# Kernel tuning notes

Measured on AMD Instinct MI355X. Metric: run time of the kernel, lower is better.

## Reference

```python
import jax, jax.numpy as jnp
import numpy as np

B, S, IN, H, D, STATE, PRED = 256, 512, 32, 256, 32, 4, 96


def setup_inputs() -> dict:
    key = jax.random.key(0)
    ks = jax.random.split(key, 16)
    sc = 1.0 / np.sqrt(H)

    def u(k, shape):
        return jax.random.uniform(k, shape, jnp.float32, -sc, sc)

    return {
        "x": jax.random.normal(ks[0], (B, S, IN), jnp.float32),
        # GRU layer 0
        "W_ih_l0": u(ks[1], (3 * H, IN)),
        "W_hh_l0": u(ks[2], (3 * H, H)),
        "b_ih_l0": u(ks[3], (3 * H,)),
        "b_hh_l0": u(ks[4], (3 * H,)),
        # GRU layer 1
        "W_ih_l1": u(ks[5], (3 * H, H)),
        "W_hh_l1": u(ks[6], (3 * H, H)),
        "b_ih_l1": u(ks[7], (3 * H,)),
        "b_hh_l1": u(ks[8], (3 * H,)),
        # state projection: hidden -> STATE*output_dim
        "W_proj": u(ks[9], (STATE * D, H)),
        "b_proj": u(ks[10], (STATE * D,)),
        # observation matrix, eye-initialized (output_dim, STATE)
        "C": jnp.eye(D, STATE, dtype=jnp.float32),
        "raw_level_decay": jnp.zeros((D,), jnp.float32),
        "raw_trend_decay": jnp.zeros((D,), jnp.float32),
        "raw_gamma": jnp.zeros((D,), jnp.float32),
        "omega": jnp.zeros((D,), jnp.float32),
    }


def _gru_layer(xs, W_ih, W_hh, b_ih, b_hh):
    # xs: (B, S, in_dim). Precompute input projections as one big GEMM.
    xp = jnp.einsum('bsi,gi->bsg', xs, W_ih) + b_ih  # (B, S, 3H)

    def step(h, xt):
        gh = h @ W_hh.T + b_hh  # (B, 3H)
        xr, xz, xn = jnp.split(xt, 3, axis=-1)
        hr, hz, hn = jnp.split(gh, 3, axis=-1)
        r = jax.nn.sigmoid(xr + hr)
        z = jax.nn.sigmoid(xz + hz)
        n = jnp.tanh(xn + r * hn)
        h_new = (1.0 - z) * n + z * h
        return h_new, h_new

    h0 = jnp.zeros((xs.shape[0], W_hh.shape[1]), xs.dtype)
    _, hs = jax.lax.scan(step, h0, jnp.swapaxes(xp, 0, 1))  # (S, B, H)
    return jnp.swapaxes(hs, 0, 1)  # (B, S, H)


def reference(x, W_ih_l0, W_hh_l0, b_ih_l0, b_hh_l0,
              W_ih_l1, W_hh_l1, b_ih_l1, b_hh_l1,
              W_proj, b_proj, C,
              raw_level_decay, raw_trend_decay, raw_gamma, omega):
    h1 = _gru_layer(x, W_ih_l0, W_hh_l0, b_ih_l0, b_hh_l0)
    h2 = _gru_layer(h1, W_ih_l1, W_hh_l1, b_ih_l1, b_hh_l1)
    final_h = h2[:, -1, :]  # (B, H)

    d_out = C.shape[0]
    s = (final_h @ W_proj.T + b_proj).reshape(x.shape[0], d_out, STATE)  # (B, D, 4)

    # time-invariant block-diagonal transition coefficients
    a_l = jax.nn.sigmoid(raw_level_decay) * 0.15 + 0.85
    a_t = jax.nn.sigmoid(raw_trend_decay) * 0.25 + 0.7
    g = jax.nn.sigmoid(raw_gamma) * 0.2 + 0.8
    c, sn = jnp.cos(omega), jnp.sin(omega)
    rot00, rot01 = g * c, -g * sn
    rot10, rot11 = g * sn, g * c

    def step(s, _):
        new_s = jnp.stack([
            s[..., 0] * a_l,
            s[..., 1] * a_t,
            s[..., 2] * rot00 + s[..., 3] * rot10,
            s[..., 2] * rot01 + s[..., 3] * rot11,
        ], axis=-1)
        y = jnp.einsum('ds,bds->bd', C, new_s)
        return new_s, y

    _, ys = jax.lax.scan(step, s, None, length=PRED)  # (PRED, B, D)
    return jnp.swapaxes(ys, 0, 1)  # (B, PRED, D)
```

## Files before the change

### kernel.cpp

```cpp
#include <hip/hip_runtime.h>
#include <cstdio>
#include <cstdint>

typedef _Float16 f16;
typedef f16 hf2   __attribute__((ext_vector_type(2)));
typedef f16 f16x8 __attribute__((ext_vector_type(8)));
typedef float f32x4 __attribute__((ext_vector_type(4)));
typedef unsigned int   u32;
typedef unsigned short u16;

#define B_    256
#define S_    512
#define IN_   32
#define H_    256
#define G3_   768
#define D_    32
#define PRED_ 96
#define TC_   32

#if __has_builtin(__builtin_amdgcn_fdot2)
__device__ __forceinline__ float fdot2(hf2 a, hf2 b, float c) {
  return __builtin_amdgcn_fdot2(a, b, c, false);
}
#else
__device__ __forceinline__ float fdot2(hf2 a, hf2 b, float c) {
  return c + (float)a[0] * (float)b[0] + (float)a[1] * (float)b[1];
}
#endif

__device__ __forceinline__ float sigm(float x) {
  return __builtin_amdgcn_rcpf(1.f + __expf(-x));
}
__device__ __forceinline__ float tanh_fast(float x) {
  return 1.f - 2.f * __builtin_amdgcn_rcpf(__expf(2.f * x) + 1.f);
}
__device__ __forceinline__ hf2 bc2(u32 v) { return __builtin_bit_cast(hf2, v); }

__global__ void f32_to_f16_k(const float* __restrict__ in, f16* __restrict__ out, int n) {
  int i = blockIdx.x * blockDim.x + threadIdx.x;
  if (i < n) out[i] = (f16)in[i];
}

__global__ void make_bias(const float* __restrict__ bih, const float* __restrict__ bhh,
                          float* __restrict__ out) {
  int i = blockIdx.x * blockDim.x + threadIdx.x;
  if (i < G3_) out[i] = bih[i] + (i < 512 ? bhh[i] : 0.f);
}

__device__ __forceinline__ f16x8 cvt8(const float* p) {
  float4 lo = ((const float4*)p)[0];
  float4 hi = ((const float4*)p)[1];
  f16x8 r;
  r[0] = (f16)lo.x; r[1] = (f16)lo.y; r[2] = (f16)lo.z; r[3] = (f16)lo.w;
  r[4] = (f16)hi.x; r[5] = (f16)hi.y; r[6] = (f16)hi.z; r[7] = (f16)hi.w;
  return r;
}

template <int KK>
__global__ __launch_bounds__(256) void gemm_xp(
    const void* __restrict__ Asrc, size_t aBlk, int tl_rows,
    const f16* __restrict__ Wih,
    const float* __restrict__ biasc,
    u16* __restrict__ xp) {
  const int tid = threadIdx.x;
  const int wv = tid >> 6, lane = tid & 63, lm = lane & 15, q = lane >> 4;
  const int tiles_pb = tl_rows >> 6;
  const int b = blockIdx.x / tiles_pb, hf = blockIdx.x % tiles_pb;
  const size_t arow0 = (size_t)b * aBlk + (size_t)(hf * 64) * KK;
  const size_t orow0 = (size_t)b * tl_rows + hf * 64;

#pragma unroll 1
  for (int nt = 0; nt < 12; ++nt) {
    const int n0 = wv * 192 + nt * 16;
    const f16* Bp = Wih + (size_t)(n0 + lm) * KK + q * 8;
    f32x4 acc[4];
#pragma unroll
    for (int j = 0; j < 4; ++j) acc[j] = f32x4{0.f, 0.f, 0.f, 0.f};
#pragma unroll
    for (int k0 = 0; k0 < KK; k0 += 32) {
      f16x8 bv = *(const f16x8*)(Bp + k0);
#pragma unroll
      for (int j = 0; j < 4; ++j) {
        f16x8 av;
        if constexpr (KK == 32) {
          av = cvt8((const float*)Asrc + arow0 + (size_t)(j * 16 + lm) * KK + k0 + q * 8);
        } else {
          av = *(const f16x8*)((const f16*)Asrc + arow0 + (size_t)(j * 16 + lm) * KK + k0 + q * 8);
        }
        acc[j] = __builtin_amdgcn_mfma_f32_16x16x32_f16(av, bv, acc[j], 0, 0, 0);
      }
    }
    const float bb = biasc[n0 + lm];
#pragma unroll
    for (int j = 0; j < 4; ++j)
#pragma unroll
      for (int r = 0; r < 4; ++r)
        xp[(orow0 + j * 16 + q * 4 + r) * G3_ + n0 + lm] =
            __builtin_bit_cast(u16, (f16)(acc[j][r] + bb));
  }
}

template <int LAYER>
__global__ __launch_bounds__(512, 2) void gru_rec(
    const u16* __restrict__ xp,
    const f16* __restrict__ Whh16,
    const float* __restrict__ bhh,
    float* __restrict__ hstate,
    f16* __restrict__ h1c,
    int tl_rows, int first) {
  const int b   = blockIdx.x;
  const int tid = threadIdx.x;
  const int p = tid >> 1, kh = tid & 1;

  uint4 w[48];
  const uint4* wsrc = (const uint4*)Whh16 + (size_t)p * 32 + kh * 16;
#pragma unroll
  for (int g = 0; g < 3; ++g)
#pragma unroll
    for (int u = 0; u < 16; ++u)
      w[g * 16 + u] = wsrc[g * 8192 + u];
  const float bhn = bhh[512 + p];

  __shared__ u16 xbuf[2][TC_ * G3_];
  __shared__ __align__(16) u16 hbuf[2][H_];
  __shared__ u16 hhist[TC_ * H_];

  float h = first ? 0.f : hstate[b * H_ + p];
  if (kh == 0) hbuf[0][p] = __builtin_bit_cast(u16, (f16)h);
  int cur = 0;
  const uint4* xsrc = (const uint4*)xp + (size_t)b * tl_rows * 96;
  const int nsub = tl_rows >> 5;

#pragma unroll 1
  for (int c2 = 0; c2 < nsub; ++c2) {
    {
      const uint4* src = xsrc + (size_t)c2 * 3072;
      uint4 v0 = src[tid],        v1 = src[512 + tid],  v2 = src[1024 + tid];
      uint4 v3 = src[1536 + tid], v4 = src[2048 + tid], v5 = src[2560 + tid];
      uint4* dst = (uint4*)xbuf[c2 & 1];
      dst[tid] = v0;        dst[512 + tid] = v1;  dst[1024 + tid] = v2;
      dst[1536 + tid] = v3; dst[2048 + tid] = v4; dst[2560 + tid] = v5;
    }
    __syncthreads();
    const u16* xrow0 = xbuf[c2 & 1];

#pragma unroll 1
    for (int tl = 0; tl < TC_; ++tl) {
      const uint4* hb = (const uint4*)(hbuf[cur] + kh * 128);
      float ar = 0.f, az = 0.f, an = 0.f, ar2 = 0.f, az2 = 0.f, an2 = 0.f;
#pragma unroll
      for (int cc = 0; cc < 16; ++cc) {
        uint4 hv = hb[cc];
        uint4 w0 = w[cc], w1 = w[16 + cc], w2 = w[32 + cc];
        ar  = fdot2(bc2(w0.x), bc2(hv.x), ar);
        az  = fdot2(bc2(w1.x), bc2(hv.x), az);
        an  = fdot2(bc2(w2.x), bc2(hv.x), an);
        ar2 = fdot2(bc2(w0.y), bc2(hv.y), ar2);
        az2 = fdot2(bc2(w1.y), bc2(hv.y), az2);
        an2 = fdot2(bc2(w2.y), bc2(hv.y), an2);
        ar  = fdot2(bc2(w0.z), bc2(hv.z), ar);
        az  = fdot2(bc2(w1.z), bc2(hv.z), az);
        an  = fdot2(bc2(w2.z), bc2(hv.z), an);
        ar2 = fdot2(bc2(w0.w), bc2(hv.w), ar2);
        az2 = fdot2(bc2(w1.w), bc2(hv.w), az2);
        an2 = fdot2(bc2(w2.w), bc2(hv.w), an2);
      }
      ar += ar2; az += az2; an += an2;
      ar += __shfl_xor(ar, 1);
      az += __shfl_xor(az, 1);
      an += __shfl_xor(an, 1);

      const u16* xrow = xrow0 + tl * G3_;
      float xr = (float)__builtin_bit_cast(f16, xrow[p]);
      float xz = (float)__builtin_bit_cast(f16, xrow[256 + p]);
      float xn = (float)__builtin_bit_cast(f16, xrow[512 + p]);
      float r = sigm(xr + ar);
      float z = sigm(xz + az);
      float n = tanh_fast(xn + r * (an + bhn));
      h = n + z * (h - n);

      if (kh == 0) {
        u16 h16v = __builtin_bit_cast(u16, (f16)h);
        hbuf[cur ^ 1][p] = h16v;
        if constexpr (LAYER == 0) hhist[tl * H_ + p] = h16v;
      }
      __syncthreads();
      cur ^= 1;
    }

    if constexpr (LAYER == 0) {
      uint4 hv0 = ((const uint4*)hhist)[tid];
      uint4 hv1 = ((const uint4*)hhist)[512 + tid];
      uint4* dst = (uint4*)(h1c + ((size_t)b * tl_rows + c2 * TC_) * H_);
      dst[tid] = hv0;
      dst[512 + tid] = hv1;
    }
  }
  if (kh == 0) hstate[b * H_ + p] = h;
}

__global__ __launch_bounds__(128) void proj_rollout(
    const float* __restrict__ hfinal, const float* __restrict__ Wp,
    const float* __restrict__ bp, const float* __restrict__ Cm,
    const float* __restrict__ rld, const float* __restrict__ rtd,
    const float* __restrict__ rg, const float* __restrict__ om,
    float* __restrict__ out) {
  const int b = blockIdx.x, tid = threadIdx.x;
  __shared__ float fh[256];
  __shared__ float sb[128];
  ((float2*)fh)[tid] = ((const float2*)(hfinal + b * 256))[tid];
  __syncthreads();
  const float4* wrow = (const float4*)(Wp + tid * 256);
  float acc = 0.f;
#pragma unroll 16
  for (int k4 = 0; k4 < 64; k4++) {
    float4 wv = wrow[k4];
    acc += wv.x * fh[4 * k4] + wv.y * fh[4 * k4 + 1] + wv.z * fh[4 * k4 + 2] +
           wv.w * fh[4 * k4 + 3];
  }
  sb[tid] = acc + bp[tid];
  __syncthreads();
  if (tid < 32) {
    const int dd = tid;
    float s0 = sb[dd * 4], s1 = sb[dd * 4 + 1], s2 = sb[dd * 4 + 2], s3 = sb[dd * 4 + 3];
    float al = sigm(rld[dd]) * 0.15f + 0.85f;
    float at = sigm(rtd[dd]) * 0.25f + 0.70f;
    float g  = sigm(rg[dd]) * 0.20f + 0.80f;
    float cw = cosf(om[dd]), sw = sinf(om[dd]);
    float r00 = g * cw, r01 = -g * sw, r10 = g * sw, r11 = g * cw;
    float c0 = Cm[dd * 4], c1 = Cm[dd * 4 + 1], c2 = Cm[dd * 4 + 2], c3 = Cm[dd * 4 + 3];
    float* op = out + (size_t)b * PRED_ * D_ + dd;
    for (int t = 0; t < PRED_; t++) {
      float n0 = s0 * al, n1 = s1 * at;
      float n2 = s2 * r00 + s3 * r10;
      float n3 = s2 * r01 + s3 * r11;
      op[(size_t)t * D_] = c0 * n0 + c1 * n1 + c2 * n2 + c3 * n3;
      s0 = n0; s1 = n1; s2 = n2; s3 = n3;
    }
  }
}

extern "C" void kernel_launch(void* const* d_in, const int* in_sizes, int n_in,
                              void* d_out, int out_size, void* d_ws,
                              size_t ws_size, hipStream_t stream) {
  (void)in_sizes; (void)n_in; (void)out_size;
  const float* x     = (const float*)d_in[0];
  const float* Wih0  = (const float*)d_in[1];
  const float* Whh0  = (const float*)d_in[2];
  const float* bih0  = (const float*)d_in[3];
  const float* bhh0  = (const float*)d_in[4];
  const float* Wih1  = (const float*)d_in[5];
  const float* Whh1  = (const float*)d_in[6];
  const float* bih1  = (const float*)d_in[7];
  const float* bhh1  = (const float*)d_in[8];
  const float* Wproj = (const float*)d_in[9];
  const float* bproj = (const float*)d_in[10];
  const float* Cm    = (const float*)d_in[11];
  const float* rld   = (const float*)d_in[12];
  const float* rtd   = (const float*)d_in[13];
  const float* rg    = (const float*)d_in[14];
  const float* om    = (const float*)d_in[15];
  float* out = (float*)d_out;

  char* ws = (char*)d_ws;
  const size_t wi0_off  = 0;
  const size_t wi1_off  = 49152;
  const size_t whh0_off = 442368;
  const size_t whh1_off = 835584;
  const size_t b0_off   = 1228800;
  const size_t b1_off   = 1231872;
  const size_t hs0_off  = 1234944;
  const size_t hs1_off  = 1497088;
  const size_t h1c_off  = 1759232;
  const size_t need64  = h1c_off + (size_t)B_ * 64 * H_ * 2  + (size_t)B_ * 64 * G3_ * 2;
  const size_t need128 = h1c_off + (size_t)B_ * 128 * H_ * 2 + (size_t)B_ * 128 * G3_ * 2;

  if (ws_size < need64) {
    fprintf(stderr, "kernel_launch: ws too small: have %zu need %zu — skipping\n",
            ws_size, need64);
    return;
  }
  const int TL = (ws_size >= need128) ? 128 : 64;
  const size_t xpc_off = h1c_off + (size_t)B_ * TL * H_ * 2;

  f16* wi016   = (f16*)(ws + wi0_off);
  f16* wi116   = (f16*)(ws + wi1_off);
  f16* whh016  = (f16*)(ws + whh0_off);
  f16* whh116  = (f16*)(ws + whh1_off);
  float* bias0 = (float*)(ws + b0_off);
  float* bias1 = (float*)(ws + b1_off);
  float* hst0  = (float*)(ws + hs0_off);
  float* hst1  = (float*)(ws + hs1_off);
  f16* h1c     = (f16*)(ws + h1c_off);
  u16* xpc     = (u16*)(ws + xpc_off);

  f32_to_f16_k<<<96, 256, 0, stream>>>(Wih0, wi016, G3_ * IN_);
  f32_to_f16_k<<<768, 256, 0, stream>>>(Wih1, wi116, G3_ * H_);
  f32_to_f16_k<<<768, 256, 0, stream>>>(Whh0, whh016, G3_ * H_);
  f32_to_f16_k<<<768, 256, 0, stream>>>(Whh1, whh116, G3_ * H_);
  make_bias<<<3, 256, 0, stream>>>(bih0, bhh0, bias0);
  make_bias<<<3, 256, 0, stream>>>(bih1, bhh1, bias1);

  const int nchunks = S_ / TL;
  const int gblocks = B_ * (TL / 64);
  for (int c = 0; c < nchunks; ++c) {
    gemm_xp<IN_><<<gblocks, 256, 0, stream>>>(
        (const void*)(x + (size_t)c * TL * IN_), (size_t)S_ * IN_, TL, wi016, bias0, xpc);
    gru_rec<0><<<B_, 512, 0, stream>>>(xpc, whh016, bhh0, hst0, h1c, TL, c == 0);
    gemm_xp<H_><<<gblocks, 256, 0, stream>>>(
        (const void*)h1c, (size_t)TL * H_, TL, wi116, bias1, xpc);
    gru_rec<1><<<B_, 512, 0, stream>>>(xpc, whh116, bhh1, hst1, nullptr, TL, c == 0);
  }
  proj_rollout<<<B_, 128, 0, stream>>>(hst1, Wproj, bproj, Cm, rld, rtd, rg, om, out);
}
```

Baseline: 1.555 ms.

## Split recurrent matvec into 4-way K slices with two outputs per thread

The GRU recurrence now gives each thread two hidden units and a quarter of the K dimension, where before it had one unit and half of K. Each h vector load from LDS now feeds six dot-product chains, so per-step LDS reads drop and instruction-level parallelism rises. The h buffer is padded to a stride of 72 to avoid LDS bank conflicts. The cost is a 4-lane shuffle reduction for six accumulators, with half the threads idle during the gate math, and the x-chunk staging loop is reorganised into two passes.

```diff
diff --git a/kernel.cpp b/kernel.cpp
--- a/kernel.cpp
+++ b/kernel.cpp
@@ -17,6 +17,7 @@
 #define D_    32
 #define PRED_ 96
 #define TC_   32
+#define KP_   72
 
 #if __has_builtin(__builtin_amdgcn_fdot2)
 __device__ __forceinline__ float fdot2(hf2 a, hf2 b, float c) {
@@ -110,23 +111,29 @@
     int tl_rows, int first) {
   const int b   = blockIdx.x;
   const int tid = threadIdx.x;
-  const int p = tid >> 1, kh = tid & 1;
-
-  uint4 w[48];
-  const uint4* wsrc = (const uint4*)Whh16 + (size_t)p * 32 + kh * 16;
+  const int p2 = tid >> 2, kh = tid & 3;
+  const int u0 = p2 * 2;
+
+  uint4 w0[3][8], w1[3][8];
 #pragma unroll
   for (int g = 0; g < 3; ++g)
 #pragma unroll
-    for (int u = 0; u < 16; ++u)
-      w[g * 16 + u] = wsrc[g * 8192 + u];
-  const float bhn = bhh[512 + p];
+    for (int t = 0; t < 8; ++t) {
+      w0[g][t] = ((const uint4*)Whh16)[(size_t)(g * 256 + u0) * 32 + kh * 8 + t];
+      w1[g][t] = ((const uint4*)Whh16)[(size_t)(g * 256 + u0 + 1) * 32 + kh * 8 + t];
+    }
+  const int myu = u0 + kh;
+  const float bhn = (kh < 2) ? bhh[512 + myu] : 0.f;
 
   __shared__ u16 xbuf[2][TC_ * G3_];
-  __shared__ __align__(16) u16 hbuf[2][H_];
+  __shared__ __align__(16) u16 hbuf[2][4 * KP_];
   __shared__ u16 hhist[TC_ * H_];
 
-  float h = first ? 0.f : hstate[b * H_ + p];
-  if (kh == 0) hbuf[0][p] = __builtin_bit_cast(u16, (f16)h);
+  float h = 0.f;
+  if (kh < 2) {
+    h = first ? 0.f : hstate[b * H_ + myu];
+    hbuf[0][(myu >> 6) * KP_ + (myu & 63)] = __builtin_bit_cast(u16, (f16)h);
+  }
   int cur = 0;
   const uint4* xsrc = (const uint4*)xp + (size_t)b * tl_rows * 96;
   const int nsub = tl_rows >> 5;
@@ -135,54 +142,76 @@
   for (int c2 = 0; c2 < nsub; ++c2) {
     {
       const uint4* src = xsrc + (size_t)c2 * 3072;
-      uint4 v0 = src[tid],        v1 = src[512 + tid],  v2 = src[1024 + tid];
-      uint4 v3 = src[1536 + tid], v4 = src[2048 + tid], v5 = src[2560 + tid];
       uint4* dst = (uint4*)xbuf[c2 & 1];
-      dst[tid] = v0;        dst[512 + tid] = v1;  dst[1024 + tid] = v2;
-      dst[1536 + tid] = v3; dst[2048 + tid] = v4; dst[2560 + tid] = v5;
+#pragma unroll
+      for (int pass = 0; pass < 2; ++pass) {
+        uint4 v0 = src[(pass * 3 + 0) * 512 + tid];
+        uint4 v1 = src[(pass * 3 + 1) * 512 + tid];
+        uint4 v2 = src[(pass * 3 + 2) * 512 + tid];
+        dst[(pass * 3 + 0) * 512 + tid] = v0;
+        dst[(pass * 3 + 1) * 512 + tid] = v1;
+        dst[(pass * 3 + 2) * 512 + tid] = v2;
+      }
     }
     __syncthreads();
     const u16* xrow0 = xbuf[c2 & 1];
 
 #pragma unroll 1
     for (int tl = 0; tl < TC_; ++tl) {
-      const uint4* hb = (const uint4*)(hbuf[cur] + kh * 128);
-      float ar = 0.f, az = 0.f, an = 0.f, ar2 = 0.f, az2 = 0.f, an2 = 0.f;
-#pragma unroll
-      for (int cc = 0; cc < 16; ++cc) {
+      const uint4* hb = (const uint4*)(hbuf[cur] + kh * KP_);
+      float a0r = 0.f, a0z = 0.f, a0n = 0.f, a1r = 0.f, a1z = 0.f, a1n = 0.f;
+#pragma unroll
+      for (int cc = 0; cc < 8; ++cc) {
         uint4 hv = hb[cc];
-        uint4 w0 = w[cc], w1 = w[16 + cc], w2 = w[32 + cc];
-        ar  = fdot2(bc2(w0.x), bc2(hv.x), ar);
-        az  = fdot2(bc2(w1.x), bc2(hv.x), az);
-        an  = fdot2(bc2(w2.x), bc2(hv.x), an);
-        ar2 = fdot2(bc2(w0.y), bc2(hv.y), ar2);
-        az2 = fdot2(bc2(w1.y), bc2(hv.y), az2);
-        an2 = fdot2(bc2(w2.y), bc2(hv.y), an2);
-        ar  = fdot2(bc2(w0.z), bc2(hv.z), ar);
-        az  = fdot2(bc2(w1.z), bc2(hv.z), az);
-        an  = fdot2(bc2(w2.z), bc2(hv.z), an);
-        ar2 = fdot2(bc2(w0.w), bc2(hv.w), ar2);
-        az2 = fdot2(bc2(w1.w), bc2(hv.w), az2);
-        an2 = fdot2(bc2(w2.w), bc2(hv.w), an2);
+        uint4 wa = w0[0][cc], wb = w0[1][cc], wc = w0[2][cc];
+        uint4 wd = w1[0][cc], we = w1[1][cc], wf = w1[2][cc];
+        a0r = fdot2(bc2(wa.x), bc2(hv.x), a0r);
+        a0z = fdot2(bc2(wb.x), bc2(hv.x), a0z);
+        a0n = fdot2(bc2(wc.x), bc2(hv.x), a0n);
+        a1r = fdot2(bc2(wd.x), bc2(hv.x), a1r);
+        a1z = fdot2(bc2(we.x), bc2(hv.x), a1z);
+        a1n = fdot2(bc2(wf.x), bc2(hv.x), a1n);
+        a0r = fdot2(bc2(wa.y), bc2(hv.y), a0r);
+        a0z = fdot2(bc2(wb.y), bc2(hv.y), a0z);
+        a0n = fdot2(bc2(wc.y), bc2(hv.y), a0n);
+        a1r = fdot2(bc2(wd.y), bc2(hv.y), a1r);
+        a1z = fdot2(bc2(we.y), bc2(hv.y), a1z);
+        a1n = fdot2(bc2(wf.y), bc2(hv.y), a1n);
+        a0r = fdot2(bc2(wa.z), bc2(hv.z), a0r);
+        a0z = fdot2(bc2(wb.z), bc2(hv.z), a0z);
+        a0n = fdot2(bc2(wc.z), bc2(hv.z), a0n);
+        a1r = fdot2(bc2(wd.z), bc2(hv.z), a1r);
+        a1z = fdot2(bc2(we.z), bc2(hv.z), a1z);
+        a1n = fdot2(bc2(wf.z), bc2(hv.z), a1n);
+        a0r = fdot2(bc2(wa.w), bc2(hv.w), a0r);
+        a0z = fdot2(bc2(wb.w), bc2(hv.w), a0z);
+        a0n = fdot2(bc2(wc.w), bc2(hv.w), a0n);
+        a1r = fdot2(bc2(wd.w), bc2(hv.w), a1r);
+        a1z = fdot2(bc2(we.w), bc2(hv.w), a1z);
+        a1n = fdot2(bc2(wf.w), bc2(hv.w), a1n);
       }
-      ar += ar2; az += az2; an += an2;
-      ar += __shfl_xor(ar, 1);
-      az += __shfl_xor(az, 1);
-      an += __shfl_xor(an, 1);
-
-      const u16* xrow = xrow0 + tl * G3_;
-      float xr = (float)__builtin_bit_cast(f16, xrow[p]);
-      float xz = (float)__builtin_bit_cast(f16, xrow[256 + p]);
-      float xn = (float)__builtin_bit_cast(f16, xrow[512 + p]);
-      float r = sigm(xr + ar);
-      float z = sigm(xz + az);
-      float n = tanh_fast(xn + r * (an + bhn));
-      h = n + z * (h - n);
-
-      if (kh == 0) {
-        u16 h16v = __builtin_bit_cast(u16, (f16)h);
-        hbuf[cur ^ 1][p] = h16v;
-        if constexpr (LAYER == 0) hhist[tl * H_ + p] = h16v;
+      a0r += __shfl_xor(a0r, 1); a0r += __shfl_xor(a0r, 2);
+      a0z += __shfl_xor(a0z, 1); a0z += __shfl_xor(a0z, 2);
+      a0n += __shfl_xor(a0n, 1); a0n += __shfl_xor(a0n, 2);
+      a1r += __shfl_xor(a1r, 1); a1r += __shfl_xor(a1r, 2);
+      a1z += __shfl_xor(a1z, 1); a1z += __shfl_xor(a1z, 2);
+      a1n += __shfl_xor(a1n, 1); a1n += __shfl_xor(a1n, 2);
+
+      if (kh < 2) {
+        const float ar = (kh == 0) ? a0r : a1r;
+        const float az = (kh == 0) ? a0z : a1z;
+        const float an = (kh == 0) ? a0n : a1n;
+        const u16* xrow = xrow0 + tl * G3_;
+        float xr = (float)__builtin_bit_cast(f16, xrow[myu]);
+        float xz = (float)__builtin_bit_cast(f16, xrow[256 + myu]);
+        float xn = (float)__builtin_bit_cast(f16, xrow[512 + myu]);
+        float r = sigm(xr + ar);
+        float z = sigm(xz + az);
+        float n = tanh_fast(xn + r * (an + bhn));
+        h = n + z * (h - n);
+        const u16 h16v = __builtin_bit_cast(u16, (f16)h);
+        hbuf[cur ^ 1][(myu >> 6) * KP_ + (myu & 63)] = h16v;
+        if constexpr (LAYER == 0) hhist[tl * H_ + myu] = h16v;
       }
       __syncthreads();
       cur ^= 1;
@@ -196,7 +225,7 @@
       dst[512 + tid] = hv1;
     }
   }
-  if (kh == 0) hstate[b * H_ + p] = h;
+  if (kh < 2) hstate[b * H_ + myu] = h;
 }
 
 __global__ __launch_bounds__(128) void proj_rollout(
```

Result: slower. 1.640 ms (+5.4%).

## Split GRU recurrence across 768 threads with gate-row partitioning and LDS exchange

Applied to the files above, without the earlier changes.

The recurrent kernel changes from 512 threads, each holding three gate rows for half of K, to 768 threads, each holding two adjacent gate rows for half of K. Partial sums are combined with a DPP lane swap and written to shared memory, and an extra barrier lets 256 threads apply the gate nonlinearities. The h buffer gets padded halves to avoid LDS bank conflicts. This aims to cut per-thread register pressure and the serial dot-product length per step, at the cost of an additional __syncthreads per timestep and threads sitting idle during the elementwise phase.

```diff
diff --git a/kernel.cpp b/kernel.cpp
--- a/kernel.cpp
+++ b/kernel.cpp
@@ -17,6 +17,7 @@
 #define D_    32
 #define PRED_ 96
 #define TC_   32
+#define HP_   136
 
 #if __has_builtin(__builtin_amdgcn_fdot2)
 __device__ __forceinline__ float fdot2(hf2 a, hf2 b, float c) {
@@ -27,6 +28,11 @@
   return c + (float)a[0] * (float)b[0] + (float)a[1] * (float)b[1];
 }
 #endif
+
+__device__ __forceinline__ float dpp_add_xor1(float x) {
+  int y = __builtin_amdgcn_mov_dpp(__builtin_bit_cast(int, x), 0xB1, 0xF, 0xF, true);
+  return x + __builtin_bit_cast(float, y);
+}
 
 __device__ __forceinline__ float sigm(float x) {
   return __builtin_amdgcn_rcpf(1.f + __expf(-x));
@@ -101,7 +107,7 @@
 }
 
 template <int LAYER>
-__global__ __launch_bounds__(512, 2) void gru_rec(
+__global__ __launch_bounds__(768, 3) void gru_rec(
     const u16* __restrict__ xp,
     const f16* __restrict__ Whh16,
     const float* __restrict__ bhh,
@@ -110,23 +116,30 @@
     int tl_rows, int first) {
   const int b   = blockIdx.x;
   const int tid = threadIdx.x;
-  const int p = tid >> 1, kh = tid & 1;
-
-  uint4 w[48];
-  const uint4* wsrc = (const uint4*)Whh16 + (size_t)p * 32 + kh * 16;
-#pragma unroll
-  for (int g = 0; g < 3; ++g)
-#pragma unroll
-    for (int u = 0; u < 16; ++u)
-      w[g * 16 + u] = wsrc[g * 8192 + u];
-  const float bhn = bhh[512 + p];
+  const int g  = tid >> 8;
+  const int i  = tid & 255;
+  const int kh = i & 1, up = i >> 1;
+  const int u0 = up * 2;
+
+  uint4 w0[16], w1[16];
+  {
+    const uint4* r0 = (const uint4*)Whh16 + (size_t)(g * 256 + u0) * 32 + kh * 16;
+    const uint4* r1 = (const uint4*)Whh16 + (size_t)(g * 256 + u0 + 1) * 32 + kh * 16;
+#pragma unroll
+    for (int t = 0; t < 16; ++t) { w0[t] = r0[t]; w1[t] = r1[t]; }
+  }
+  const float bhn = (tid < 256) ? bhh[512 + tid] : 0.f;
 
   __shared__ u16 xbuf[2][TC_ * G3_];
-  __shared__ __align__(16) u16 hbuf[2][H_];
+  __shared__ __align__(16) u16 hbuf[2][2 * HP_];
+  __shared__ float pa[G3_];
   __shared__ u16 hhist[TC_ * H_];
 
-  float h = first ? 0.f : hstate[b * H_ + p];
-  if (kh == 0) hbuf[0][p] = __builtin_bit_cast(u16, (f16)h);
+  float h = 0.f;
+  if (tid < 256) {
+    h = first ? 0.f : hstate[b * H_ + tid];
+    hbuf[0][(tid >> 7) * HP_ + (tid & 127)] = __builtin_bit_cast(u16, (f16)h);
+  }
   int cur = 0;
   const uint4* xsrc = (const uint4*)xp + (size_t)b * tl_rows * 96;
   const int nsub = tl_rows >> 5;
@@ -135,68 +148,70 @@
   for (int c2 = 0; c2 < nsub; ++c2) {
     {
       const uint4* src = xsrc + (size_t)c2 * 3072;
-      uint4 v0 = src[tid],        v1 = src[512 + tid],  v2 = src[1024 + tid];
-      uint4 v3 = src[1536 + tid], v4 = src[2048 + tid], v5 = src[2560 + tid];
       uint4* dst = (uint4*)xbuf[c2 & 1];
-      dst[tid] = v0;        dst[512 + tid] = v1;  dst[1024 + tid] = v2;
-      dst[1536 + tid] = v3; dst[2048 + tid] = v4; dst[2560 + tid] = v5;
+#pragma unroll
+      for (int pass = 0; pass < 2; ++pass) {
+        uint4 v0 = src[(pass * 2 + 0) * 768 + tid];
+        uint4 v1 = src[(pass * 2 + 1) * 768 + tid];
+        dst[(pass * 2 + 0) * 768 + tid] = v0;
+        dst[(pass * 2 + 1) * 768 + tid] = v1;
+      }
     }
     __syncthreads();
     const u16* xrow0 = xbuf[c2 & 1];
 
 #pragma unroll 1
     for (int tl = 0; tl < TC_; ++tl) {
-      const uint4* hb = (const uint4*)(hbuf[cur] + kh * 128);
-      float ar = 0.f, az = 0.f, an = 0.f, ar2 = 0.f, az2 = 0.f, an2 = 0.f;
+      const uint4* hb = (const uint4*)(hbuf[cur] + kh * HP_);
+      float a0 = 0.f, a1 = 0.f, a0b = 0.f, a1b = 0.f;
 #pragma unroll
       for (int cc = 0; cc < 16; ++cc) {
         uint4 hv = hb[cc];
-        uint4 w0 = w[cc], w1 = w[16 + cc], w2 = w[32 + cc];
-        ar  = fdot2(bc2(w0.x), bc2(hv.x), ar);
-        az  = fdot2(bc2(w1.x), bc2(hv.x), az);
-        an  = fdot2(bc2(w2.x), bc2(hv.x), an);
-        ar2 = fdot2(bc2(w0.y), bc2(hv.y), ar2);
-        az2 = fdot2(bc2(w1.y), bc2(hv.y), az2);
-        an2 = fdot2(bc2(w2.y), bc2(hv.y), an2);
-        ar  = fdot2(bc2(w0.z), bc2(hv.z), ar);
-        az  = fdot2(bc2(w1.z), bc2(hv.z), az);
-        an  = fdot2(bc2(w2.z), bc2(hv.z), an);
-        ar2 = fdot2(bc2(w0.w), bc2(hv.w), ar2);
-        az2 = fdot2(bc2(w1.w), bc2(hv.w), az2);
-        an2 = fdot2(bc2(w2.w), bc2(hv.w), an2);
-      }
-      ar += ar2; az += az2; an += an2;
-      ar += __shfl_xor(ar, 1);
-      az += __shfl_xor(az, 1);
-      an += __shfl_xor(an, 1);
-
-      const u16* xrow = xrow0 + tl * G3_;
-      float xr = (float)__builtin_bit_cast(f16, xrow[p]);
-      float xz = (float)__builtin_bit_cast(f16, xrow[256 + p]);
-      float xn = (float)__builtin_bit_cast(f16, xrow[512 + p]);
-      float r = sigm(xr + ar);
-      float z = sigm(xz + az);
-      float n = tanh_fast(xn + r * (an + bhn));
-      h = n + z * (h - n);
-
-      if (kh == 0) {
-        u16 h16v = __builtin_bit_cast(u16, (f16)h);
-        hbuf[cur ^ 1][p] = h16v;
-        if constexpr (LAYER == 0) hhist[tl * H_ + p] = h16v;
+        uint4 wa = w0[cc], wb = w1[cc];
+        a0  = fdot2(bc2(wa.x), bc2(hv.x), a0);
+        a1  = fdot2(bc2(wb.x), bc2(hv.x), a1);
+        a0b = fdot2(bc2(wa.y), bc2(hv.y), a0b);
+        a1b = fdot2(bc2(wb.y), bc2(hv.y), a1b);
+        a0  = fdot2(bc2(wa.z), bc2(hv.z), a0);
+        a1  = fdot2(bc2(wb.z), bc2(hv.z), a1);
+        a0b = fdot2(bc2(wa.w), bc2(hv.w), a0b);
+        a1b = fdot2(bc2(wb.w), bc2(hv.w), a1b);
+      }
+      a0 += a0b; a1 += a1b;
+      a0 = dpp_add_xor1(a0);
+      a1 = dpp_add_xor1(a1);
+      pa[tid] = kh ? a1 : a0;
+      __syncthreads();
+
+      if (tid < 256) {
+        const int u = tid;
+        const u16* xrow = xrow0 + tl * G3_;
+        float xr = (float)__builtin_bit_cast(f16, xrow[u]);
+        float xz = (float)__builtin_bit_cast(f16, xrow[256 + u]);
+        float xn = (float)__builtin_bit_cast(f16, xrow[512 + u]);
+        float r = sigm(xr + pa[u]);
+        float z = sigm(xz + pa[256 + u]);
+        float n = tanh_fast(xn + r * (pa[512 + u] + bhn));
+        h = n + z * (h - n);
+        const u16 h16v = __builtin_bit_cast(u16, (f16)h);
+        hbuf[cur ^ 1][(u >> 7) * HP_ + (u & 127)] = h16v;
+        if constexpr (LAYER == 0) hhist[tl * H_ + u] = h16v;
       }
       __syncthreads();
       cur ^= 1;
     }
 
     if constexpr (LAYER == 0) {
-      uint4 hv0 = ((const uint4*)hhist)[tid];
-      uint4 hv1 = ((const uint4*)hhist)[512 + tid];
-      uint4* dst = (uint4*)(h1c + ((size_t)b * tl_rows + c2 * TC_) * H_);
-      dst[tid] = hv0;
-      dst[512 + tid] = hv1;
-    }
-  }
-  if (kh == 0) hstate[b * H_ + p] = h;
+      if (tid < 512) {
+        uint4 hv0 = ((const uint4*)hhist)[tid];
+        uint4 hv1 = ((const uint4*)hhist)[512 + tid];
+        uint4* dst = (uint4*)(h1c + ((size_t)b * tl_rows + c2 * TC_) * H_);
+        dst[tid] = hv0;
+        dst[512 + tid] = hv1;
+      }
+    }
+  }
+  if (tid < 256) hstate[b * H_ + tid] = h;
 }
 
 __global__ __launch_bounds__(128) void proj_rollout(
@@ -306,10 +321,10 @@
   for (int c = 0; c < nchunks; ++c) {
     gemm_xp<IN_><<<gblocks, 256, 0, stream>>>(
         (const void*)(x + (size_t)c * TL * IN_), (size_t)S_ * IN_, TL, wi016, bias0, xpc);
-    gru_rec<0><<<B_, 512, 0, stream>>>(xpc, whh016, bhh0, hst0, h1c, TL, c == 0);
+    gru_rec<0><<<B_, 768, 0, stream>>>(xpc, whh016, bhh0, hst0, h1c, TL, c == 0);
     gemm_xp<H_><<<gblocks, 256, 0, stream>>>(
         (const void*)h1c, (size_t)TL * H_, TL, wi116, bias1, xpc);
-    gru_rec<1><<<B_, 512, 0, stream>>>(xpc, whh116, bhh1, hst1, nullptr, TL, c == 0);
+    gru_rec<1><<<B_, 768, 0, stream>>>(xpc, whh116, bhh1, hst1, nullptr, TL, c == 0);
   }
   proj_rollout<<<B_, 128, 0, stream>>>(hst1, Wproj, bproj, Cm, rld, rtd, rg, om, out);
 }
```

After: 1.546 ms. No clear change (-0.6%).
